# Kernel optimization log

Hardware: AMD Instinct MI355X
Metric: run time of the kernel (lower is better)

The kernel has to match this reference:

```python
import jax, jax.numpy as jnp
import numpy as np

N, E, C, D, H = 50000, 1600000, 50000, 128, 512


def setup_inputs() -> dict:
    key = jax.random.key(0)
    ks = jax.random.split(key, 16)
    s = jnp.float32(0.02)  # keep activations stable through 3 layers
    inp = {}
    inp["x"] = jax.random.normal(ks[0], (N, D), jnp.float32)
    inp["edge_index"] = jax.random.randint(ks[1], (2, E), 0, N)
    inp["first_edge"] = jax.random.randint(ks[2], (2,), 0, N)
    inp["candidate_edges"] = jax.random.randint(ks[3], (C, 2), 0, N)
    inp["t"] = jax.random.uniform(ks[4], (1, 1), jnp.float32)
    dims = [(D, H), (H, H), (H, H)]
    i = 5
    for l, (di, do) in enumerate(dims):
        inp[f"gin{l}_w1"] = jax.random.normal(ks[i], (di, do), jnp.float32) * s; i += 1
        inp[f"gin{l}_b1"] = jnp.zeros((do,), jnp.float32)
        inp[f"gin{l}_w2"] = jax.random.normal(ks[i], (do, do), jnp.float32) * s; i += 1
        inp[f"gin{l}_b2"] = jnp.zeros((do,), jnp.float32)
    inp["pred_w1"] = jax.random.normal(ks[i], (5 * H, H), jnp.float32) * s; i += 1
    inp["pred_b1"] = jnp.zeros((H,), jnp.float32)
    inp["pred_w2"] = jax.random.normal(ks[i], (H, 1), jnp.float32) * s; i += 1
    inp["pred_b2"] = jnp.zeros((1,), jnp.float32)
    inp["time_w1"] = jax.random.normal(ks[i], (1, H), jnp.float32) * s; i += 1
    inp["time_b1"] = jnp.zeros((H,), jnp.float32)
    inp["time_w2"] = jax.random.normal(ks[i], (H, H), jnp.float32) * s; i += 1
    inp["time_b2"] = jnp.zeros((H,), jnp.float32)
    return inp


def _edge_rep(x, u, v):
    # 'sum_absdiff': cat([x_u + x_v, |x_u - x_v|]) -> 2*H features
    xu, xv = x[u], x[v]
    return jnp.concatenate([xu + xv, jnp.abs(xu - xv)], axis=-1)


def reference(x, edge_index, first_edge, candidate_edges, t,
              gin0_w1, gin0_b1, gin0_w2, gin0_b2,
              gin1_w1, gin1_b1, gin1_w2, gin1_b2,
              gin2_w1, gin2_b1, gin2_w2, gin2_b2,
              pred_w1, pred_b1, pred_w2, pred_b2,
              time_w1, time_b1, time_w2, time_b2):
    src, dst = edge_index[0], edge_index[1]
    layers = [(gin0_w1, gin0_b1, gin0_w2, gin0_b2),
              (gin1_w1, gin1_b1, gin1_w2, gin1_b2),
              (gin2_w1, gin2_b1, gin2_w2, gin2_b2)]
    # GINConv (eps=0): h_i = MLP(x_i + sum_{j->i} x_j)
    for w1, b1, w2, b2 in layers:
        agg = jax.ops.segment_sum(x[src], dst, num_segments=x.shape[0])
        h = x + agg
        x = jax.nn.relu(h @ w1 + b1) @ w2 + b2
    first_feat = _edge_rep(x, first_edge[0], first_edge[1])  # [2H]
    t_embed = (jax.nn.relu(t @ time_w1 + time_b1) @ time_w2 + time_b2)[0]  # [H]
    cand_feat = _edge_rep(x, candidate_edges[:, 0], candidate_edges[:, 1])  # [C, 2H]
    Cn = cand_feat.shape[0]
    feat = jnp.concatenate([
        jnp.broadcast_to(first_feat, (Cn, first_feat.shape[0])),
        cand_feat,
        jnp.broadcast_to(t_embed, (Cn, t_embed.shape[0])),
    ], axis=-1)  # [C, 5H]
    logits = (jax.nn.relu(feat @ pred_w1 + pred_b1) @ pred_w2 + pred_b2)[:, 0]  # [C]
    return logits
```

## Files before the change

kernel.cpp:

```cpp
#include <hip/hip_runtime.h>

typedef __bf16 bf16x2 __attribute__((ext_vector_type(2)));
typedef __bf16 bf16x4 __attribute__((ext_vector_type(4)));
typedef __bf16 bf16x8 __attribute__((ext_vector_type(8)));
typedef float f32x4 __attribute__((ext_vector_type(4)));

#define LDSTR 40

__global__ void hist_kernel(const int* __restrict__ dst, int* __restrict__ deg, int E) {
    int i = blockIdx.x * 256 + threadIdx.x;
    if (i < E) atomicAdd(&deg[dst[i]], 1);
}

__global__ __launch_bounds__(256)
void blocksum_kernel(const int* __restrict__ deg, int* __restrict__ bsum, int n) {
    __shared__ int red[256];
    int i = blockIdx.x * 256 + threadIdx.x;
    red[threadIdx.x] = (i < n) ? deg[i] : 0;
    __syncthreads();
    for (int off = 128; off > 0; off >>= 1) {
        if (threadIdx.x < off) red[threadIdx.x] += red[threadIdx.x + off];
        __syncthreads();
    }
    if (threadIdx.x == 0) bsum[blockIdx.x] = red[0];
}

__global__ __launch_bounds__(256)
void scanb_kernel(int* __restrict__ bsum, int nb) {
    __shared__ int s[256];
    int t = threadIdx.x;
    s[t] = (t < nb) ? bsum[t] : 0;
    __syncthreads();
    for (int off = 1; off < 256; off <<= 1) {
        int v = (t >= off) ? s[t - off] : 0;
        __syncthreads();
        s[t] += v;
        __syncthreads();
    }
    if (t < nb) bsum[t] = (t == 0) ? 0 : s[t - 1];
}

__global__ __launch_bounds__(256)
void scanw_kernel(const int* __restrict__ deg, const int* __restrict__ bsum,
                  int* __restrict__ rowptr, int* __restrict__ cursor, int n) {
    __shared__ int s[256];
    int b = blockIdx.x, t = threadIdx.x;
    int i = b * 256 + t;
    int d = (i < n) ? deg[i] : 0;
    s[t] = d;
    __syncthreads();
    for (int off = 1; off < 256; off <<= 1) {
        int v = (t >= off) ? s[t - off] : 0;
        __syncthreads();
        s[t] += v;
        __syncthreads();
    }
    int incl = s[t];
    int base = bsum[b];
    if (i < n) {
        int r = base + incl - d;
        rowptr[i] = r;
        cursor[i] = r;
        if (i == n - 1) rowptr[n] = base + incl;
    }
}

__global__ void scatter_kernel(const int* __restrict__ src, const int* __restrict__ dst,
                               int* __restrict__ cursor, int* __restrict__ colsrc, int E) {
    int i = blockIdx.x * 256 + threadIdx.x;
    if (i < E) {
        int p = atomicAdd(&cursor[dst[i]], 1);
        colsrc[p] = src[i];
    }
}

__global__ void f32_to_bf16_kernel(const float* __restrict__ in, __bf16* __restrict__ out, int n4) {
    int i = blockIdx.x * 256 + threadIdx.x;
    if (i < n4) {
        float4 f = ((const float4*)in)[i];
        bf16x4 o;
        o[0] = (__bf16)f.x; o[1] = (__bf16)f.y; o[2] = (__bf16)f.z; o[3] = (__bf16)f.w;
        ((bf16x4*)out)[i] = o;
    }
}

__global__ void wprep_kernel(const float* __restrict__ in, __bf16* __restrict__ out, int kbits) {
    int idx = blockIdx.x * 256 + threadIdx.x;
    int K = 1 << kbits;
    if (idx < (512 << kbits)) {
        int k = idx & (K - 1);
        int n = idx >> kbits;
        out[idx] = (__bf16)in[k * 512 + n];
    }
}

template<int F> struct VecT;
template<> struct VecT<2> { using T = bf16x2; };
template<> struct VecT<4> { using T = bf16x4; };
template<> struct VecT<8> { using T = bf16x8; };

template<int F, int U, int STR>
__global__ __launch_bounds__(256)
void agg_kernel(const __bf16* __restrict__ xb, const int* __restrict__ rowptr,
                const int* __restrict__ colsrc, __bf16* __restrict__ h, int n, int colbase) {
    const int node = blockIdx.x * 4 + (threadIdx.x >> 6);
    if (node >= n) return;
    const int lane = threadIdx.x & 63;
    using V = typename VecT<F>::T;

    const __bf16* xl = xb + colbase + lane * F;

    float acc[F];
    {
        V v = *(const V*)(xl + (size_t)node * STR);
        #pragma unroll
        for (int i = 0; i < F; i++) acc[i] = (float)v[i];
    }

    int e   = __builtin_amdgcn_readfirstlane(rowptr[node]);
    int end = __builtin_amdgcn_readfirstlane(rowptr[node + 1]);

    for (; e + U <= end; e += U) {
        int s[U];
        #pragma unroll
        for (int j = 0; j < U; j++) s[j] = colsrc[e + j];
        V v[U];
        #pragma unroll
        for (int j = 0; j < U; j++) v[j] = *(const V*)(xl + (size_t)s[j] * STR);
        #pragma unroll
        for (int j = 0; j < U; j++)
            #pragma unroll
            for (int i = 0; i < F; i++) acc[i] += (float)v[j][i];
    }
    if constexpr (U > 4) {
        for (; e + 4 <= end; e += 4) {
            int s[4];
            #pragma unroll
            for (int j = 0; j < 4; j++) s[j] = colsrc[e + j];
            V v[4];
            #pragma unroll
            for (int j = 0; j < 4; j++) v[j] = *(const V*)(xl + (size_t)s[j] * STR);
            #pragma unroll
            for (int j = 0; j < 4; j++)
                #pragma unroll
                for (int i = 0; i < F; i++) acc[i] += (float)v[j][i];
        }
    }
    for (; e < end; e++) {
        int s0 = colsrc[e];
        V v = *(const V*)(xl + (size_t)s0 * STR);
        #pragma unroll
        for (int i = 0; i < F; i++) acc[i] += (float)v[i];
    }

    __bf16* out = h + colbase + (size_t)node * STR + lane * F;
    V o;
    #pragma unroll
    for (int i = 0; i < F; i++) o[i] = (__bf16)acc[i];
    *(V*)out = o;
}

template<int AMODE, bool RELU>
__global__ __launch_bounds__(256, 3)
void gemm_kernel(const __bf16* __restrict__ A, const __bf16* __restrict__ Xb,
                 const int* __restrict__ cand, const __bf16* __restrict__ Bt,
                 const float* __restrict__ bias, __bf16* __restrict__ Cout,
                 int M, int K) {
    __shared__ __bf16 sA[64 * LDSTR];
    __shared__ __bf16 sB[256 * LDSTR];

    const int tid = threadIdx.x;
    const int lane = tid & 63;
    const int waveN = tid >> 6;
    const int mlane = lane & 15;
    const int quad = lane >> 4;
    const int rowBase = blockIdx.x * 64;
    const int nBase = blockIdx.y * 256;

    const int ar = tid >> 2;
    const int ac = (tid & 3) << 3;
    const int br = tid >> 2;
    const int bc = (tid & 3) << 3;

    const f32x4 fzero = {0.f, 0.f, 0.f, 0.f};
    f32x4 acc[4][4];
    #pragma unroll
    for (int i = 0; i < 4; i++)
        #pragma unroll
        for (int j = 0; j < 4; j++) acc[i][j] = fzero;

    int uu = 0, vv = 0;
    const int grow = rowBase + ar;
    if (AMODE == 1 && grow < M) { uu = cand[2 * grow]; vv = cand[2 * grow + 1]; }

    for (int k0 = 0; k0 < K; k0 += 32) {
        __syncthreads();
        {
            bf16x8 av = {};
            if (AMODE == 0) {
                if (grow < M) av = *(const bf16x8*)(A + (size_t)grow * K + k0 + ac);
            } else {
                if (grow < M) {
                    int k = k0 + ac;
                    int kk = k & 511;
                    bf16x8 xu = *(const bf16x8*)(Xb + (size_t)uu * 512 + kk);
                    bf16x8 xv = *(const bf16x8*)(Xb + (size_t)vv * 512 + kk);
                    if (k < 512) {
                        #pragma unroll
                        for (int q = 0; q < 8; q++) av[q] = (__bf16)((float)xu[q] + (float)xv[q]);
                    } else {
                        #pragma unroll
                        for (int q = 0; q < 8; q++) av[q] = (__bf16)fabsf((float)xu[q] - (float)xv[q]);
                    }
                }
            }
            *(bf16x8*)(sA + ar * LDSTR + ac) = av;
        }
        #pragma unroll
        for (int i = 0; i < 4; i++) {
            int nn = br + i * 64;
            bf16x8 b = *(const bf16x8*)(Bt + (size_t)(nBase + nn) * K + k0 + bc);
            *(bf16x8*)(sB + nn * LDSTR + bc) = b;
        }
        __syncthreads();

        bf16x8 aF[4], bF[4];
        #pragma unroll
        for (int mt = 0; mt < 4; mt++)
            aF[mt] = *(const bf16x8*)(sA + (mt * 16 + mlane) * LDSTR + quad * 8);
        #pragma unroll
        for (int nt = 0; nt < 4; nt++)
            bF[nt] = *(const bf16x8*)(sB + (waveN * 64 + nt * 16 + mlane) * LDSTR + quad * 8);
        #pragma unroll
        for (int mt = 0; mt < 4; mt++)
            #pragma unroll
            for (int nt = 0; nt < 4; nt++)
                acc[mt][nt] = __builtin_amdgcn_mfma_f32_16x16x32_bf16(aF[mt], bF[nt], acc[mt][nt], 0, 0, 0);
    }

    #pragma unroll
    for (int mt = 0; mt < 4; mt++) {
        #pragma unroll
        for (int nt = 0; nt < 4; nt++) {
            int col = nBase + waveN * 64 + nt * 16 + mlane;
            float bv = bias[col];
            #pragma unroll
            for (int r = 0; r < 4; r++) {
                int row = rowBase + mt * 16 + quad * 4 + r;
                if (row < M) {
                    float v = acc[mt][nt][r] + bv;
                    if (RELU) v = fmaxf(v, 0.f);
                    Cout[(size_t)row * 512 + col] = (__bf16)v;
                }
            }
        }
    }
}

__global__ __launch_bounds__(512)
void constvec_kernel(const __bf16* __restrict__ xb, const int* __restrict__ first_edge,
                     const float* __restrict__ t,
                     const float* __restrict__ tw1, const float* __restrict__ tb1,
                     const float* __restrict__ tw2, const float* __restrict__ tb2,
                     const float* __restrict__ pw1, const float* __restrict__ pb1,
                     float* __restrict__ cvec) {
    __shared__ float z1[512];
    __shared__ float te[512];
    __shared__ float ff[1024];
    int tid = threadIdx.x;
    float tv = t[0];
    z1[tid] = fmaxf(tv * tw1[tid] + tb1[tid], 0.f);
    int u = first_edge[0], v = first_edge[1];
    float xu = (float)xb[(size_t)u * 512 + tid];
    float xv = (float)xb[(size_t)v * 512 + tid];
    ff[tid] = xu + xv;
    ff[512 + tid] = fabsf(xu - xv);
    __syncthreads();
    float s = tb2[tid];
    for (int j = 0; j < 512; j++) s += z1[j] * tw2[j * 512 + tid];
    te[tid] = s;
    __syncthreads();
    float c = pb1[tid];
    for (int k = 0; k < 1024; k++) c += ff[k] * pw1[k * 512 + tid];
    for (int j = 0; j < 512; j++) c += te[j] * pw1[(2048 + j) * 512 + tid];
    cvec[tid] = c;
}

__global__ __launch_bounds__(256)
void logits_kernel(const __bf16* __restrict__ Z, const float* __restrict__ w2,
                   const float* __restrict__ b2, float* __restrict__ out, int C) {
    int c = blockIdx.x * 4 + (threadIdx.x >> 6);
    if (c >= C) return;
    int lane = threadIdx.x & 63;
    bf16x8 z = *(const bf16x8*)(Z + (size_t)c * 512 + lane * 8);
    const float4* w = (const float4*)(w2 + lane * 8);
    float4 w0 = w[0], w1 = w[1];
    float s = (float)z[0] * w0.x + (float)z[1] * w0.y + (float)z[2] * w0.z + (float)z[3] * w0.w
            + (float)z[4] * w1.x + (float)z[5] * w1.y + (float)z[6] * w1.z + (float)z[7] * w1.w;
    #pragma unroll
    for (int off = 32; off > 0; off >>= 1) s += __shfl_down(s, off);
    if (lane == 0) out[c] = s + b2[0];
}

extern "C" void kernel_launch(void* const* d_in, const int* in_sizes, int n_in,
                              void* d_out, int out_size, void* d_ws, size_t ws_size,
                              hipStream_t stream) {
    (void)n_in; (void)out_size; (void)ws_size;
    const float* x          = (const float*)d_in[0];
    const int*   edge_index = (const int*)d_in[1];
    const int*   first_edge = (const int*)d_in[2];
    const int*   cand       = (const int*)d_in[3];
    const float* t          = (const float*)d_in[4];
    const float* gw1[3] = {(const float*)d_in[5], (const float*)d_in[9],  (const float*)d_in[13]};
    const float* gb1[3] = {(const float*)d_in[6], (const float*)d_in[10], (const float*)d_in[14]};
    const float* gw2[3] = {(const float*)d_in[7], (const float*)d_in[11], (const float*)d_in[15]};
    const float* gb2[3] = {(const float*)d_in[8], (const float*)d_in[12], (const float*)d_in[16]};
    const float* pw1 = (const float*)d_in[17];
    const float* pb1 = (const float*)d_in[18];
    const float* pw2 = (const float*)d_in[19];
    const float* pb2 = (const float*)d_in[20];
    const float* tw1 = (const float*)d_in[21];
    const float* tb1 = (const float*)d_in[22];
    const float* tw2 = (const float*)d_in[23];
    const float* tb2 = (const float*)d_in[24];

    const int N = in_sizes[0] / 128;
    const int E = in_sizes[1] / 2;
    const int C = in_sizes[3] / 2;

    char* p = (char*)d_ws;
    auto alloc = [&](size_t bytes) -> void* {
        void* r = (void*)p;
        p += (bytes + 255) & ~(size_t)255;
        return r;
    };
    __bf16* h    = (__bf16*)alloc((size_t)N * 512 * 2);
    __bf16* u    = (__bf16*)alloc((size_t)N * 512 * 2);
    __bf16* xb   = (__bf16*)alloc((size_t)N * 512 * 2);
    __bf16* wt01 = (__bf16*)alloc((size_t)512 * 128 * 2);
    __bf16* wt02 = (__bf16*)alloc((size_t)512 * 512 * 2);
    __bf16* wt11 = (__bf16*)alloc((size_t)512 * 512 * 2);
    __bf16* wt12 = (__bf16*)alloc((size_t)512 * 512 * 2);
    __bf16* wt21 = (__bf16*)alloc((size_t)512 * 512 * 2);
    __bf16* wt22 = (__bf16*)alloc((size_t)512 * 512 * 2);
    __bf16* wtH  = (__bf16*)alloc((size_t)512 * 1024 * 2);
    int* rowptr = (int*)alloc((size_t)(N + 1) * 4);
    int* deg    = (int*)alloc((size_t)N * 4);
    int* cursor = (int*)alloc((size_t)N * 4);
    int* colsrc = (int*)alloc((size_t)E * 4);
    int* bsum   = (int*)alloc((size_t)256 * 4);
    float* cvec = (float*)alloc(512 * 4);
    __bf16* xb0 = (__bf16*)u;

    const int* src = edge_index;
    const int* dst = edge_index + E;

    hipMemsetAsync(deg, 0, (size_t)N * 4, stream);
    int eb = (E + 255) / 256;
    int nb = (N + 255) / 256;
    hist_kernel<<<eb, 256, 0, stream>>>(dst, deg, E);
    blocksum_kernel<<<nb, 256, 0, stream>>>(deg, bsum, N);
    scanb_kernel<<<1, 256, 0, stream>>>(bsum, nb);
    scanw_kernel<<<nb, 256, 0, stream>>>(deg, bsum, rowptr, cursor, N);
    scatter_kernel<<<eb, 256, 0, stream>>>(src, dst, cursor, colsrc, E);

    f32_to_bf16_kernel<<<((N * 128 / 4) + 255) / 256, 256, 0, stream>>>(x, xb0, N * 128 / 4);
    wprep_kernel<<<((512 << 7)  + 255) / 256, 256, 0, stream>>>(gw1[0], wt01, 7);
    wprep_kernel<<<((512 << 9)  + 255) / 256, 256, 0, stream>>>(gw2[0], wt02, 9);
    wprep_kernel<<<((512 << 9)  + 255) / 256, 256, 0, stream>>>(gw1[1], wt11, 9);
    wprep_kernel<<<((512 << 9)  + 255) / 256, 256, 0, stream>>>(gw2[1], wt12, 9);
    wprep_kernel<<<((512 << 9)  + 255) / 256, 256, 0, stream>>>(gw1[2], wt21, 9);
    wprep_kernel<<<((512 << 9)  + 255) / 256, 256, 0, stream>>>(gw2[2], wt22, 9);
    wprep_kernel<<<((512 << 10) + 255) / 256, 256, 0, stream>>>(pw1 + (size_t)1024 * 512, wtH, 10);

    dim3 ggrid((N + 63) / 64, 2);
    int ablocks = (N + 3) / 4;

    agg_kernel<2, 16, 128><<<ablocks, 256, 0, stream>>>(xb0, rowptr, colsrc, h, N, 0);
    gemm_kernel<0, true ><<<ggrid, 256, 0, stream>>>(h, nullptr, nullptr, wt01, gb1[0], u,  N, 128);
    gemm_kernel<0, false><<<ggrid, 256, 0, stream>>>(u, nullptr, nullptr, wt02, gb2[0], xb, N, 512);
    agg_kernel<4, 8, 512><<<ablocks, 256, 0, stream>>>(xb, rowptr, colsrc, h, N, 0);
    agg_kernel<4, 8, 512><<<ablocks, 256, 0, stream>>>(xb, rowptr, colsrc, h, N, 256);
    gemm_kernel<0, true ><<<ggrid, 256, 0, stream>>>(h, nullptr, nullptr, wt11, gb1[1], u,  N, 512);
    gemm_kernel<0, false><<<ggrid, 256, 0, stream>>>(u, nullptr, nullptr, wt12, gb2[1], xb, N, 512);
    agg_kernel<4, 8, 512><<<ablocks, 256, 0, stream>>>(xb, rowptr, colsrc, h, N, 0);
    agg_kernel<4, 8, 512><<<ablocks, 256, 0, stream>>>(xb, rowptr, colsrc, h, N, 256);
    gemm_kernel<0, true ><<<ggrid, 256, 0, stream>>>(h, nullptr, nullptr, wt21, gb1[2], u,  N, 512);
    gemm_kernel<0, false><<<ggrid, 256, 0, stream>>>(u, nullptr, nullptr, wt22, gb2[2], xb, N, 512);

    constvec_kernel<<<1, 512, 0, stream>>>(xb, first_edge, t, tw1, tb1, tw2, tb2, pw1, pb1, cvec);
    dim3 hgrid((C + 63) / 64, 2);
    gemm_kernel<1, true><<<hgrid, 256, 0, stream>>>(nullptr, xb, cand, wtH, cvec, u, C, 1024);
    logits_kernel<<<(C + 3) / 4, 256, 0, stream>>>(u, pw2, pb2, (float*)d_out, C);
}
```

Baseline: 1.300 ms.

## Double-buffer GEMM shared-memory tiles with register prefetch of next K-slice

The GEMM main loop now keeps two shared-memory buffers for the A and B tiles. It issues the global loads for the next K-slice into registers before running the MFMAs on the current buffer, then writes those registers into the other buffer. This hides global-load latency behind the matrix math and cuts the syncs per iteration from two to one. In exchange it doubles LDS usage (about 50KB) and adds prefetch registers, which may lower occupancy under the launch bound of 3 blocks.

```diff
diff --git a/kernel.cpp b/kernel.cpp
--- a/kernel.cpp
+++ b/kernel.cpp
@@ -166,8 +166,8 @@
                  const int* __restrict__ cand, const __bf16* __restrict__ Bt,
                  const float* __restrict__ bias, __bf16* __restrict__ Cout,
                  int M, int K) {
-    __shared__ __bf16 sA[64 * LDSTR];
-    __shared__ __bf16 sB[256 * LDSTR];
+    __shared__ __bf16 sA[2][64 * LDSTR];
+    __shared__ __bf16 sB[2][256 * LDSTR];
 
     const int tid = threadIdx.x;
     const int lane = tid & 63;
@@ -179,8 +179,6 @@
 
     const int ar = tid >> 2;
     const int ac = (tid & 3) << 3;
-    const int br = tid >> 2;
-    const int bc = (tid & 3) << 3;
 
     const f32x4 fzero = {0.f, 0.f, 0.f, 0.f};
     f32x4 acc[4][4];
@@ -191,51 +189,79 @@
 
     int uu = 0, vv = 0;
     const int grow = rowBase + ar;
-    if (AMODE == 1 && grow < M) { uu = cand[2 * grow]; vv = cand[2 * grow + 1]; }
-
-    for (int k0 = 0; k0 < K; k0 += 32) {
-        __syncthreads();
-        {
-            bf16x8 av = {};
-            if (AMODE == 0) {
-                if (grow < M) av = *(const bf16x8*)(A + (size_t)grow * K + k0 + ac);
-            } else {
-                if (grow < M) {
-                    int k = k0 + ac;
-                    int kk = k & 511;
-                    bf16x8 xu = *(const bf16x8*)(Xb + (size_t)uu * 512 + kk);
-                    bf16x8 xv = *(const bf16x8*)(Xb + (size_t)vv * 512 + kk);
-                    if (k < 512) {
-                        #pragma unroll
-                        for (int q = 0; q < 8; q++) av[q] = (__bf16)((float)xu[q] + (float)xv[q]);
-                    } else {
-                        #pragma unroll
-                        for (int q = 0; q < 8; q++) av[q] = (__bf16)fabsf((float)xu[q] - (float)xv[q]);
-                    }
+    const bool arowok = (grow < M);
+    if (AMODE == 1 && arowok) { uu = cand[2 * grow]; vv = cand[2 * grow + 1]; }
+
+    bf16x8 pa{}, pxu{}, pxv{};
+    bf16x8 pb[4];
+    int pk = 0;
+
+    auto issue = [&](int k0) {
+        pk = k0;
+        if (AMODE == 0) {
+            pa = {};
+            if (arowok) pa = *(const bf16x8*)(A + (size_t)grow * K + k0 + ac);
+        } else {
+            if (arowok) {
+                int kk = (k0 + ac) & 511;
+                pxu = *(const bf16x8*)(Xb + (size_t)uu * 512 + kk);
+                pxv = *(const bf16x8*)(Xb + (size_t)vv * 512 + kk);
+            }
+        }
+        #pragma unroll
+        for (int i = 0; i < 4; i++)
+            pb[i] = *(const bf16x8*)(Bt + (size_t)(nBase + ar + i * 64) * K + k0 + ac);
+    };
+
+    auto commit = [&](int buf) {
+        bf16x8 av;
+        if (AMODE == 0) {
+            av = pa;
+        } else {
+            av = bf16x8{};
+            if (arowok) {
+                if (pk + ac < 512) {
+                    #pragma unroll
+                    for (int q = 0; q < 8; q++) av[q] = (__bf16)((float)pxu[q] + (float)pxv[q]);
+                } else {
+                    #pragma unroll
+                    for (int q = 0; q < 8; q++) av[q] = (__bf16)fabsf((float)pxu[q] - (float)pxv[q]);
                 }
             }
-            *(bf16x8*)(sA + ar * LDSTR + ac) = av;
         }
-        #pragma unroll
-        for (int i = 0; i < 4; i++) {
-            int nn = br + i * 64;
-            bf16x8 b = *(const bf16x8*)(Bt + (size_t)(nBase + nn) * K + k0 + bc);
-            *(bf16x8*)(sB + nn * LDSTR + bc) = b;
-        }
-        __syncthreads();
+        *(bf16x8*)(sA[buf] + ar * LDSTR + ac) = av;
+        #pragma unroll
+        for (int i = 0; i < 4; i++)
+            *(bf16x8*)(sB[buf] + (ar + i * 64) * LDSTR + ac) = pb[i];
+    };
+
+    issue(0);
+    commit(0);
+    __syncthreads();
+
+    int cur = 0;
+    for (int k0 = 0; k0 < K; k0 += 32) {
+        const bool more = (k0 + 32 < K);
+        if (more) issue(k0 + 32);
 
         bf16x8 aF[4], bF[4];
         #pragma unroll
         for (int mt = 0; mt < 4; mt++)
-            aF[mt] = *(const bf16x8*)(sA + (mt * 16 + mlane) * LDSTR + quad * 8);
+            aF[mt] = *(const bf16x8*)(sA[cur] + (mt * 16 + mlane) * LDSTR + quad * 8);
         #pragma unroll
         for (int nt = 0; nt < 4; nt++)
-            bF[nt] = *(const bf16x8*)(sB + (waveN * 64 + nt * 16 + mlane) * LDSTR + quad * 8);
+            bF[nt] = *(const bf16x8*)(sB[cur] + (waveN * 64 + nt * 16 + mlane) * LDSTR + quad * 8);
         #pragma unroll
         for (int mt = 0; mt < 4; mt++)
             #pragma unroll
             for (int nt = 0; nt < 4; nt++)
                 acc[mt][nt] = __builtin_amdgcn_mfma_f32_16x16x32_bf16(aF[mt], bF[nt], acc[mt][nt], 0, 0, 0);
+
+        if (more) {
+            commit(cur ^ 1);
+            __syncthreads();
+            cur ^= 1;
+        }
     }
 
     #pragma unroll
```

After: 1.346 ms. 3.5% more time.
